# Kernel tuning notes

Measured on AMD Instinct MI355X. Metric: run time of the kernel, lower is better.

## Reference

```python
import jax, jax.numpy as jnp
import numpy as np

N, R, E, DIN, DOUT = 100000, 4, 160000, 128, 128
NEG_SLOPE = 0.2


def setup_inputs() -> dict:
    key = jax.random.key(0)
    ks = jax.random.split(key, 9)
    s_in = 1.0 / np.sqrt(DIN)
    x = jax.random.normal(ks[0], (N, DIN), jnp.float32)
    edge_src = jax.random.randint(ks[1], (R, E), 0, N)
    edge_dst = jax.random.randint(ks[2], (R, E), 0, N)
    # per-relation GATConv params (num_heads=1): fc_src, fc_dst, attn_l, attn_r, bias
    W_src = jax.random.normal(ks[3], (R, DIN, DOUT), jnp.float32) * s_in
    W_dst = jax.random.normal(ks[4], (R, DIN, DOUT), jnp.float32) * s_in
    attn_l = jax.random.normal(ks[5], (R, DOUT), jnp.float32) * 0.1
    attn_r = jax.random.normal(ks[6], (R, DOUT), jnp.float32) * 0.1
    gat_bias = jax.random.normal(ks[7], (R, DOUT), jnp.float32) * 0.01
    h_bias = jnp.zeros((DOUT,), jnp.float32)
    return {"x": x, "edge_src": edge_src, "edge_dst": edge_dst,
            "W_src": W_src, "W_dst": W_dst, "attn_l": attn_l,
            "attn_r": attn_r, "gat_bias": gat_bias, "h_bias": h_bias}


def reference(x, edge_src, edge_dst, W_src, W_dst, attn_l, attn_r, gat_bias, h_bias):
    n = x.shape[0]
    r, e = edge_src.shape
    # per-relation linear projections (GATConv fc_src / fc_dst, no bias)
    hs = jnp.einsum('nd,rde->rne', x, W_src)            # [R,N,D] source messages
    hd = jnp.einsum('nd,rde->rne', x, W_dst)            # [R,N,D] dst attn features
    el = jnp.sum(hs * attn_l[:, None, :], axis=-1)      # [R,N]
    er = jnp.sum(hd * attn_r[:, None, :], axis=-1)      # [R,N]
    rid = jnp.arange(r)[:, None]                        # [R,1]
    # edge attention logits
    logits = jax.nn.leaky_relu(
        jnp.take_along_axis(el, edge_src, axis=1)
        + jnp.take_along_axis(er, edge_dst, axis=1), NEG_SLOPE)  # [R,E]
    # edge softmax grouped by (relation, dst node): flatten into R*N segments
    seg = (edge_dst + rid * n).reshape(-1)              # [R*E]
    lf = logits.reshape(-1)
    m = jax.ops.segment_max(lf, seg, num_segments=r * n)
    a = jnp.exp(lf - m[seg])
    denom = jax.ops.segment_sum(a, seg, num_segments=r * n)
    alpha = a / denom[seg]                              # segment-normalized, denom>=1 at max edge
    msg = alpha[:, None] * hs[rid, edge_src].reshape(r * e, -1)  # [R*E,D]
    agg = jax.ops.segment_sum(msg, seg, num_segments=r * n).reshape(r, n, -1)
    agg = agg + gat_bias[:, None, :]                    # GATConv bias per relation
    h = agg.sum(0) + h_bias                             # HeteroGraphConv 'sum' + h_bias
    return jax.nn.relu(h)                               # activation; dropout eval = id; mean over 1 head = squeeze
```

## Files before the change

### kernel.cpp

```cpp
#include <hip/hip_runtime.h>
#include <hip/hip_bf16.h>

#define N_NODES 100000
#define R_REL 4
#define E_EDGES 160000
#define D 128
#define NEG_SLOPE 0.2f
#define CAP 32

typedef unsigned short u16x8 __attribute__((ext_vector_type(8)));
typedef unsigned short u16x4 __attribute__((ext_vector_type(4)));
typedef __bf16 bf16x8v __attribute__((ext_vector_type(8)));
typedef float f32x4 __attribute__((ext_vector_type(4)));

__device__ inline unsigned short f2bf(float f) {
    unsigned u = __float_as_uint(f);
    return (unsigned short)((u + 0x7FFFu + ((u >> 16) & 1u)) >> 16);
}
__device__ inline float bf2f(unsigned short h) {
    return __uint_as_float(((unsigned)h) << 16);
}

__global__ __launch_bounds__(512) void k_prep2(const float* __restrict__ Wsrc,
        const float* __restrict__ Wdst, const float* __restrict__ al,
        const float* __restrict__ ar, const float* __restrict__ gb,
        const float* __restrict__ hb, float* __restrict__ wl,
        float* __restrict__ wr, float* __restrict__ btot,
        unsigned short* __restrict__ Wt, unsigned* __restrict__ cnt) {
    int b = blockIdx.x, t = threadIdx.x;
    if (b == 0) {
        int r = t >> 7, d = t & 127;
        const float* as = al + r * D;
        const float* ad = ar + r * D;
        const float* rs = Wsrc + (r * D + d) * D;
        const float* rd = Wdst + (r * D + d) * D;
        float s0 = 0.f, s1 = 0.f;
        for (int e = 0; e < D; e++) { s0 += rs[e] * as[e]; s1 += rd[e] * ad[e]; }
        wl[r * D + d] = s0; wr[r * D + d] = s1;
        if (t < D) {
            float bb = hb[t];
            for (int r2 = 0; r2 < R_REL; r2++) bb += gb[r2 * D + t];
            btot[t] = bb;
        }
    } else if (b <= 32) {
        int base = (b - 1) * 2048 + t;
        #pragma unroll
        for (int i = 0; i < 4; i++) {
            int idx = base + i * 512;
            int r = idx >> 14; int rem = idx & 16383; int e = rem >> 7; int k = rem & 127;
            Wt[idx] = f2bf(Wsrc[(r * D + k) * D + e]);
        }
    } else {
        int i = (b - 33) * 512 + t;
        if (i < N_NODES) cnt[i] = 0u;
    }
}

__global__ __launch_bounds__(256) void k_scores_cast(const float* __restrict__ x,
        const float* __restrict__ wl, const float* __restrict__ wr,
        unsigned short* __restrict__ xb, float* __restrict__ el, float* __restrict__ er) {
    __shared__ float swl[R_REL * D], swr[R_REL * D];
    int t = threadIdx.x;
    for (int i = t; i < R_REL * D; i += 256) { swl[i] = wl[i]; swr[i] = wr[i]; }
    __syncthreads();
    int wv = t >> 6, lane = t & 63;
    int half = lane >> 5, q = lane & 31;
    long n = (long)blockIdx.x * 8 + wv * 2 + half;
    float4 v = ((const float4*)(x + n * D))[q];
    u16x4 ov;
    ov[0] = f2bf(v.x); ov[1] = f2bf(v.y); ov[2] = f2bf(v.z); ov[3] = f2bf(v.w);
    *(u16x4*)(xb + n * D + q * 4) = ov;
    float accl[R_REL], accr[R_REL];
    #pragma unroll
    for (int r = 0; r < R_REL; r++) {
        float4 w = ((const float4*)(swl + r * D))[q];
        accl[r] = v.x * w.x + v.y * w.y + v.z * w.z + v.w * w.w;
        float4 u = ((const float4*)(swr + r * D))[q];
        accr[r] = v.x * u.x + v.y * u.y + v.z * u.z + v.w * u.w;
    }
    #pragma unroll
    for (int r = 0; r < R_REL; r++) {
        #pragma unroll
        for (int d = 16; d >= 1; d >>= 1) {
            accl[r] += __shfl_xor(accl[r], d);
            accr[r] += __shfl_xor(accr[r], d);
        }
    }
    if (q == 0) {
        #pragma unroll
        for (int r = 0; r < R_REL; r++) {
            el[r * N_NODES + n] = accl[r];
            er[r * N_NODES + n] = accr[r];
        }
    }
}

__global__ __launch_bounds__(512) void k_gemm(const unsigned short* __restrict__ xb,
                                              const unsigned short* __restrict__ Wt,
                                              unsigned short* __restrict__ hs) {
    __shared__ unsigned short B[D][D + 8];
    int tid = threadIdx.x;
    int w = tid >> 6, l = tid & 63;
    int row16 = l & 15, kgrp = l >> 4;
    int r = blockIdx.y;
    int n0 = blockIdx.x * 256;
    bf16x8v a[2][4];
    int nr[2];
    #pragma unroll
    for (int rf = 0; rf < 2; rf++) {
        int nrow = n0 + w * 32 + rf * 16 + row16;
        nr[rf] = nrow;
        int nc = nrow < N_NODES ? nrow : N_NODES - 1;
        #pragma unroll
        for (int kf = 0; kf < 4; kf++)
            a[rf][kf] = *(const bf16x8v*)(xb + (long)nc * D + kf * 32 + kgrp * 8);
    }
    const unsigned short* Wr = Wt + r * D * D;
    #pragma unroll
    for (int it = 0; it < 4; it++) {
        int fi = (it * 512 + tid) * 8;
        *(u16x8*)(&B[fi >> 7][fi & 127]) = *(const u16x8*)(Wr + fi);
    }
    __syncthreads();
    f32x4 acc[2][8];
    #pragma unroll
    for (int rf = 0; rf < 2; rf++)
        #pragma unroll
        for (int et = 0; et < 8; et++) {
            acc[rf][et][0] = 0.f; acc[rf][et][1] = 0.f;
            acc[rf][et][2] = 0.f; acc[rf][et][3] = 0.f;
        }
    #pragma unroll
    for (int kf = 0; kf < 4; kf++) {
        #pragma unroll
        for (int et = 0; et < 8; et++) {
            bf16x8v av = *(const bf16x8v*)(&B[et * 16 + row16][kf * 32 + kgrp * 8]);
            acc[0][et] = __builtin_amdgcn_mfma_f32_16x16x32_bf16(av, a[0][kf], acc[0][et], 0, 0, 0);
            acc[1][et] = __builtin_amdgcn_mfma_f32_16x16x32_bf16(av, a[1][kf], acc[1][et], 0, 0, 0);
        }
    }
    #pragma unroll
    for (int rf = 0; rf < 2; rf++) {
        if (nr[rf] < N_NODES) {
            unsigned short* orow = hs + ((long)r * N_NODES + nr[rf]) * D;
            #pragma unroll
            for (int et = 0; et < 8; et++) {
                u16x4 o;
                o[0] = f2bf(acc[rf][et][0]); o[1] = f2bf(acc[rf][et][1]);
                o[2] = f2bf(acc[rf][et][2]); o[3] = f2bf(acc[rf][et][3]);
                *(u16x4*)(orow + et * 16 + kgrp * 4) = o;
            }
        }
    }
}

__global__ void k_scatter(const int* __restrict__ esrc, const int* __restrict__ edst,
                          const float* __restrict__ el, const float* __restrict__ er,
                          unsigned* __restrict__ cnt, int2* __restrict__ eb) {
    int e = blockIdx.x * 256 + threadIdx.x;
    if (e >= E_EDGES) return;
    int r = blockIdx.y;
    int t = r * E_EDGES + e;
    int src = esrc[t], dst = edst[t];
    float lg = el[r * N_NODES + src] + er[r * N_NODES + dst];
    lg = lg > 0.f ? lg : NEG_SLOPE * lg;
    float p = __expf(lg);
    unsigned pos = atomicAdd(cnt + dst, 1u);
    if (pos < CAP) eb[dst * CAP + pos] = make_int2(r * N_NODES + src, __float_as_int(p));
}

__global__ __launch_bounds__(256) void k_agg(const int2* __restrict__ eb,
                                             const unsigned* __restrict__ cnt,
                                             const unsigned short* __restrict__ hs,
                                             const float* __restrict__ btot,
                                             float* __restrict__ out) {
    int wv = threadIdx.x >> 6, lane = threadIdx.x & 63;
    int half = lane >> 5, l32 = lane & 31;
    int dst = blockIdx.x * 8 + wv * 2 + half;
    unsigned num = cnt[dst];
    if (num > CAP) num = CAP;
    int rowid = 0, r = 0;
    float p = 0.f;
    if (l32 < num) {
        int2 m = eb[dst * CAP + l32];
        rowid = m.x;
        p = __int_as_float(m.y);
        r = (int)((unsigned)rowid / (unsigned)N_NODES);
    }
    float denom[R_REL];
    #pragma unroll
    for (int rr = 0; rr < R_REL; rr++) {
        float v = (r == rr) ? p : 0.f;
        #pragma unroll
        for (int d = 1; d < 32; d <<= 1) v += __shfl_xor(v, d, 32);
        denom[rr] = v;
    }
    float alpha = (l32 < num) ? p / denom[r] : 0.f;
    int slot2 = l32 >> 4, c16 = lane & 15;
    float acc[8] = {0.f, 0.f, 0.f, 0.f, 0.f, 0.f, 0.f, 0.f};
    unsigned numo = __shfl_xor(num, 32);
    unsigned numMax = num > numo ? num : numo;
    unsigned iters = (numMax + 1) >> 1;
    for (unsigned i = 0; i < iters; i++) {
        unsigned q = slot2 + i * 2;
        int src = half * 32 + (int)q;
        int rid = __shfl(rowid, src);
        float al = __shfl(alpha, src);
        if (q < num) {
            u16x8 v = *(const u16x8*)(hs + (long)rid * D + c16 * 8);
            #pragma unroll
            for (int j = 0; j < 8; j++) acc[j] += al * bf2f(v[j]);
        }
    }
    #pragma unroll
    for (int j = 0; j < 8; j++) acc[j] += __shfl_xor(acc[j], 16);
    if (slot2 == 0) {
        const float4 b0 = *(const float4*)(btot + c16 * 8);
        const float4 b1 = *(const float4*)(btot + c16 * 8 + 4);
        float4 o0, o1;
        o0.x = acc[0] + b0.x; o0.y = acc[1] + b0.y; o0.z = acc[2] + b0.z; o0.w = acc[3] + b0.w;
        o1.x = acc[4] + b1.x; o1.y = acc[5] + b1.y; o1.z = acc[6] + b1.z; o1.w = acc[7] + b1.w;
        o0.x = o0.x > 0.f ? o0.x : 0.f; o0.y = o0.y > 0.f ? o0.y : 0.f;
        o0.z = o0.z > 0.f ? o0.z : 0.f; o0.w = o0.w > 0.f ? o0.w : 0.f;
        o1.x = o1.x > 0.f ? o1.x : 0.f; o1.y = o1.y > 0.f ? o1.y : 0.f;
        o1.z = o1.z > 0.f ? o1.z : 0.f; o1.w = o1.w > 0.f ? o1.w : 0.f;
        *(float4*)(out + (long)dst * D + c16 * 8) = o0;
        *(float4*)(out + (long)dst * D + c16 * 8 + 4) = o1;
    }
}

extern "C" void kernel_launch(void* const* d_in, const int* in_sizes, int n_in,
                              void* d_out, int out_size, void* d_ws, size_t ws_size,
                              hipStream_t stream) {
    const float* x    = (const float*)d_in[0];
    const int*   esrc = (const int*)d_in[1];
    const int*   edst = (const int*)d_in[2];
    const float* Wsrc = (const float*)d_in[3];
    const float* Wdst = (const float*)d_in[4];
    const float* al   = (const float*)d_in[5];
    const float* ar   = (const float*)d_in[6];
    const float* gb   = (const float*)d_in[7];
    const float* hb   = (const float*)d_in[8];
    float* out = (float*)d_out;

    char* ws = (char*)d_ws;
    size_t o = 0;
    auto alloc = [&](size_t bytes) -> char* {
        char* r = ws + o; o += (bytes + 255) & ~(size_t)255; return r;
    };
    unsigned short* xb  = (unsigned short*)alloc((size_t)N_NODES * D * 2);
    unsigned short* hsb = (unsigned short*)alloc((size_t)R_REL * N_NODES * D * 2);
    unsigned short* Wt  = (unsigned short*)alloc((size_t)R_REL * D * D * 2);
    float* el   = (float*)alloc((size_t)R_REL * N_NODES * 4);
    float* er   = (float*)alloc((size_t)R_REL * N_NODES * 4);
    float* wl   = (float*)alloc(R_REL * D * 4);
    float* wr   = (float*)alloc(R_REL * D * 4);
    float* btot = (float*)alloc(D * 4);
    unsigned* cnt = (unsigned*)alloc((size_t)N_NODES * 4);
    int2* eb = (int2*)xb;

    int zblocks = (N_NODES + 511) / 512;
    k_prep2<<<dim3(33 + zblocks), dim3(512), 0, stream>>>(Wsrc, Wdst, al, ar, gb, hb,
                                                          wl, wr, btot, Wt, cnt);
    k_scores_cast<<<dim3(N_NODES / 8), dim3(256), 0, stream>>>(x, wl, wr, xb, el, er);
    k_gemm<<<dim3((N_NODES + 255) / 256, R_REL), dim3(512), 0, stream>>>(xb, Wt, hsb);
    k_scatter<<<dim3((E_EDGES + 255) / 256, R_REL), dim3(256), 0, stream>>>(esrc, edst, el, er, cnt, eb);
    k_agg<<<dim3(N_NODES / 8), dim3(256), 0, stream>>>(eb, cnt, hsb, btot, out);
}
```

Before: 174.3 us.

## Fuse GEMM and edge scatter into one launch with a separate edge buffer

```diff
diff --git a/kernel.cpp b/kernel.cpp
--- a/kernel.cpp
+++ b/kernel.cpp
@@ -7,6 +7,8 @@
 #define D 128
 #define NEG_SLOPE 0.2f
 #define CAP 32
+#define GB 391
+#define SB 313
 
 typedef unsigned short u16x8 __attribute__((ext_vector_type(8)));
 typedef unsigned short u16x4 __attribute__((ext_vector_type(4)));
@@ -95,15 +97,12 @@
     }
 }
 
-__global__ __launch_bounds__(512) void k_gemm(const unsigned short* __restrict__ xb,
-                                              const unsigned short* __restrict__ Wt,
-                                              unsigned short* __restrict__ hs) {
-    __shared__ unsigned short B[D][D + 8];
-    int tid = threadIdx.x;
+__device__ __forceinline__ void gemm_body(int bx, int r, int tid,
+        const unsigned short* __restrict__ xb, const unsigned short* __restrict__ Wt,
+        unsigned short* __restrict__ hs, unsigned short (*B)[D + 8]) {
     int w = tid >> 6, l = tid & 63;
     int row16 = l & 15, kgrp = l >> 4;
-    int r = blockIdx.y;
-    int n0 = blockIdx.x * 256;
+    int n0 = bx * 256;
     bf16x8v a[2][4];
     int nr[2];
     #pragma unroll
@@ -154,12 +153,10 @@
     }
 }
 
-__global__ void k_scatter(const int* __restrict__ esrc, const int* __restrict__ edst,
-                          const float* __restrict__ el, const float* __restrict__ er,
-                          unsigned* __restrict__ cnt, int2* __restrict__ eb) {
-    int e = blockIdx.x * 256 + threadIdx.x;
-    if (e >= E_EDGES) return;
-    int r = blockIdx.y;
+__device__ __forceinline__ void scatter_edge(int e, int r,
+        const int* __restrict__ esrc, const int* __restrict__ edst,
+        const float* __restrict__ el, const float* __restrict__ er,
+        unsigned* __restrict__ cnt, int2* __restrict__ eb) {
     int t = r * E_EDGES + e;
     int src = esrc[t], dst = edst[t];
     float lg = el[r * N_NODES + src] + er[r * N_NODES + dst];
@@ -167,6 +164,37 @@
     float p = __expf(lg);
     unsigned pos = atomicAdd(cnt + dst, 1u);
     if (pos < CAP) eb[dst * CAP + pos] = make_int2(r * N_NODES + src, __float_as_int(p));
+}
+
+__global__ __launch_bounds__(512) void k_gemm_scatter(
+        const unsigned short* __restrict__ xb, const unsigned short* __restrict__ Wt,
+        unsigned short* __restrict__ hs, const int* __restrict__ esrc,
+        const int* __restrict__ edst, const float* __restrict__ el,
+        const float* __restrict__ er, unsigned* __restrict__ cnt,
+        int2* __restrict__ eb) {
+    __shared__ unsigned short B[D][D + 8];
+    int bx = blockIdx.x, r = blockIdx.y, tid = threadIdx.x;
+    if (bx < GB) {
+        gemm_body(bx, r, tid, xb, Wt, hs, B);
+    } else {
+        int e = (bx - GB) * 512 + tid;
+        if (e < E_EDGES) scatter_edge(e, r, esrc, edst, el, er, cnt, eb);
+    }
+}
+
+__global__ __launch_bounds__(512) void k_gemm(const unsigned short* __restrict__ xb,
+                                              const unsigned short* __restrict__ Wt,
+                                              unsigned short* __restrict__ hs) {
+    __shared__ unsigned short B[D][D + 8];
+    gemm_body(blockIdx.x, blockIdx.y, threadIdx.x, xb, Wt, hs, B);
+}
+
+__global__ void k_scatter(const int* __restrict__ esrc, const int* __restrict__ edst,
+                          const float* __restrict__ el, const float* __restrict__ er,
+                          unsigned* __restrict__ cnt, int2* __restrict__ eb) {
+    int e = blockIdx.x * 256 + threadIdx.x;
+    if (e >= E_EDGES) return;
+    scatter_edge(e, blockIdx.y, esrc, edst, el, er, cnt, eb);
 }
 
 __global__ __launch_bounds__(256) void k_agg(const int2* __restrict__ eb,
@@ -203,9 +231,9 @@
     unsigned iters = (numMax + 1) >> 1;
     for (unsigned i = 0; i < iters; i++) {
         unsigned q = slot2 + i * 2;
-        int src = half * 32 + (int)q;
-        int rid = __shfl(rowid, src);
-        float al = __shfl(alpha, src);
+        int srcl = half * 32 + (int)q;
+        int rid = __shfl(rowid, srcl);
+        float al = __shfl(alpha, srcl);
         if (q < num) {
             u16x8 v = *(const u16x8*)(hs + (long)rid * D + c16 * 8);
             #pragma unroll
@@ -257,13 +285,22 @@
     float* wr   = (float*)alloc(R_REL * D * 4);
     float* btot = (float*)alloc(D * 4);
     unsigned* cnt = (unsigned*)alloc((size_t)N_NODES * 4);
-    int2* eb = (int2*)xb;
+    size_t base_end = o;
+    size_t eb_bytes = (size_t)N_NODES * CAP * 8;
+    bool fused = (base_end + eb_bytes) <= ws_size;
+    int2* eb = fused ? (int2*)alloc(eb_bytes) : (int2*)xb;
 
     int zblocks = (N_NODES + 511) / 512;
     k_prep2<<<dim3(33 + zblocks), dim3(512), 0, stream>>>(Wsrc, Wdst, al, ar, gb, hb,
                                                           wl, wr, btot, Wt, cnt);
     k_scores_cast<<<dim3(N_NODES / 8), dim3(256), 0, stream>>>(x, wl, wr, xb, el, er);
-    k_gemm<<<dim3((N_NODES + 255) / 256, R_REL), dim3(512), 0, stream>>>(xb, Wt, hsb);
-    k_scatter<<<dim3((E_EDGES + 255) / 256, R_REL), dim3(256), 0, stream>>>(esrc, edst, el, er, cnt, eb);
+    if (fused) {
+        k_gemm_scatter<<<dim3(GB + SB, R_REL), dim3(512), 0, stream>>>(
+            xb, Wt, hsb, esrc, edst, el, er, cnt, eb);
+    } else {
+        k_gemm<<<dim3(GB, R_REL), dim3(512), 0, stream>>>(xb, Wt, hsb);
+        k_scatter<<<dim3((E_EDGES + 255) / 256, R_REL), dim3(256), 0, stream>>>(
+            esrc, edst, el, er, cnt, eb);
+    }
     k_agg<<<dim3(N_NODES / 8), dim3(256), 0, stream>>>(eb, cnt, hsb, btot, out);
 }
```

Measured after the change: 156.8 us. 1.11x faster.

## Aggregate raw features per relation then project, removing the per-relation GEMM

Applied to the files above, without the earlier changes.

```diff
diff --git a/kernel.cpp b/kernel.cpp
--- a/kernel.cpp
+++ b/kernel.cpp
@@ -7,6 +7,7 @@
 #define D 128
 #define NEG_SLOPE 0.2f
 #define CAP 32
+#define NB_DST 16
 
 typedef unsigned short u16x8 __attribute__((ext_vector_type(8)));
 typedef unsigned short u16x4 __attribute__((ext_vector_type(4)));
@@ -95,65 +96,6 @@
     }
 }
 
-__global__ __launch_bounds__(512) void k_gemm(const unsigned short* __restrict__ xb,
-                                              const unsigned short* __restrict__ Wt,
-                                              unsigned short* __restrict__ hs) {
-    __shared__ unsigned short B[D][D + 8];
-    int tid = threadIdx.x;
-    int w = tid >> 6, l = tid & 63;
-    int row16 = l & 15, kgrp = l >> 4;
-    int r = blockIdx.y;
-    int n0 = blockIdx.x * 256;
-    bf16x8v a[2][4];
-    int nr[2];
-    #pragma unroll
-    for (int rf = 0; rf < 2; rf++) {
-        int nrow = n0 + w * 32 + rf * 16 + row16;
-        nr[rf] = nrow;
-        int nc = nrow < N_NODES ? nrow : N_NODES - 1;
-        #pragma unroll
-        for (int kf = 0; kf < 4; kf++)
-            a[rf][kf] = *(const bf16x8v*)(xb + (long)nc * D + kf * 32 + kgrp * 8);
-    }
-    const unsigned short* Wr = Wt + r * D * D;
-    #pragma unroll
-    for (int it = 0; it < 4; it++) {
-        int fi = (it * 512 + tid) * 8;
-        *(u16x8*)(&B[fi >> 7][fi & 127]) = *(const u16x8*)(Wr + fi);
-    }
-    __syncthreads();
-    f32x4 acc[2][8];
-    #pragma unroll
-    for (int rf = 0; rf < 2; rf++)
-        #pragma unroll
-        for (int et = 0; et < 8; et++) {
-            acc[rf][et][0] = 0.f; acc[rf][et][1] = 0.f;
-            acc[rf][et][2] = 0.f; acc[rf][et][3] = 0.f;
-        }
-    #pragma unroll
-    for (int kf = 0; kf < 4; kf++) {
-        #pragma unroll
-        for (int et = 0; et < 8; et++) {
-            bf16x8v av = *(const bf16x8v*)(&B[et * 16 + row16][kf * 32 + kgrp * 8]);
-            acc[0][et] = __builtin_amdgcn_mfma_f32_16x16x32_bf16(av, a[0][kf], acc[0][et], 0, 0, 0);
-            acc[1][et] = __builtin_amdgcn_mfma_f32_16x16x32_bf16(av, a[1][kf], acc[1][et], 0, 0, 0);
-        }
-    }
-    #pragma unroll
-    for (int rf = 0; rf < 2; rf++) {
-        if (nr[rf] < N_NODES) {
-            unsigned short* orow = hs + ((long)r * N_NODES + nr[rf]) * D;
-            #pragma unroll
-            for (int et = 0; et < 8; et++) {
-                u16x4 o;
-                o[0] = f2bf(acc[rf][et][0]); o[1] = f2bf(acc[rf][et][1]);
-                o[2] = f2bf(acc[rf][et][2]); o[3] = f2bf(acc[rf][et][3]);
-                *(u16x4*)(orow + et * 16 + kgrp * 4) = o;
-            }
-        }
-    }
-}
-
 __global__ void k_scatter(const int* __restrict__ esrc, const int* __restrict__ edst,
                           const float* __restrict__ el, const float* __restrict__ er,
                           unsigned* __restrict__ cnt, int2* __restrict__ eb) {
@@ -169,64 +111,104 @@
     if (pos < CAP) eb[dst * CAP + pos] = make_int2(r * N_NODES + src, __float_as_int(p));
 }
 
-__global__ __launch_bounds__(256) void k_agg(const int2* __restrict__ eb,
-                                             const unsigned* __restrict__ cnt,
-                                             const unsigned short* __restrict__ hs,
-                                             const float* __restrict__ btot,
-                                             float* __restrict__ out) {
-    int wv = threadIdx.x >> 6, lane = threadIdx.x & 63;
+__global__ __launch_bounds__(256) void k_aggproj(
+        const int2* __restrict__ eb, const unsigned* __restrict__ cnt,
+        const unsigned short* __restrict__ xb, const unsigned short* __restrict__ Wt,
+        const float* __restrict__ btot, float* __restrict__ out) {
+    __shared__ unsigned short Z[R_REL][NB_DST][D + 8];
+    int tid = threadIdx.x;
+    int wv = tid >> 6, lane = tid & 63;
     int half = lane >> 5, l32 = lane & 31;
-    int dst = blockIdx.x * 8 + wv * 2 + half;
-    unsigned num = cnt[dst];
-    if (num > CAP) num = CAP;
-    int rowid = 0, r = 0;
-    float p = 0.f;
-    if (l32 < num) {
+    int slot2 = l32 >> 4, c16 = lane & 15;
+    int dbase = blockIdx.x * NB_DST;
+    for (int ps = 0; ps < 2; ps++) {
+        int dloc = wv * 4 + ps * 2 + half;
+        int dst = dbase + dloc;
         int2 m = eb[dst * CAP + l32];
-        rowid = m.x;
-        p = __int_as_float(m.y);
-        r = (int)((unsigned)rowid / (unsigned)N_NODES);
-    }
-    float denom[R_REL];
+        unsigned num = cnt[dst];
+        if (num > CAP) num = CAP;
+        bool live = (unsigned)l32 < num;
+        int rowid = live ? m.x : 0;
+        float pv = live ? __int_as_float(m.y) : 0.f;
+        int r = live ? (int)((unsigned)rowid / (unsigned)N_NODES) : 0;
+        float denom[R_REL];
+        #pragma unroll
+        for (int rr = 0; rr < R_REL; rr++) {
+            float v = (r == rr) ? pv : 0.f;
+            #pragma unroll
+            for (int d = 1; d < 32; d <<= 1) v += __shfl_xor(v, d, 32);
+            denom[rr] = v;
+        }
+        float alpha = live ? pv / denom[r] : 0.f;
+        float accz[R_REL][8];
+        #pragma unroll
+        for (int rr = 0; rr < R_REL; rr++)
+            #pragma unroll
+            for (int j = 0; j < 8; j++) accz[rr][j] = 0.f;
+        unsigned numo = __shfl_xor(num, 32);
+        unsigned numMax = num > numo ? num : numo;
+        unsigned iters = (numMax + 1) >> 1;
+        for (unsigned i = 0; i < iters; i++) {
+            unsigned q = slot2 + i * 2;
+            int srcl = half * 32 + (int)q;
+            int rid = __shfl(rowid, srcl);
+            float al = __shfl(alpha, srcl);
+            if (q < num) {
+                unsigned rr_e = (unsigned)rid / (unsigned)N_NODES;
+                int sidx = rid - (int)(rr_e * (unsigned)N_NODES);
+                u16x8 v = *(const u16x8*)(xb + (long)sidx * D + c16 * 8);
+                #pragma unroll
+                for (int rr = 0; rr < R_REL; rr++) {
+                    float alc = (rr_e == (unsigned)rr) ? al : 0.f;
+                    #pragma unroll
+                    for (int j = 0; j < 8; j++) accz[rr][j] += alc * bf2f(v[j]);
+                }
+            }
+        }
+        #pragma unroll
+        for (int rr = 0; rr < R_REL; rr++)
+            #pragma unroll
+            for (int j = 0; j < 8; j++) accz[rr][j] += __shfl_xor(accz[rr][j], 16);
+        if (slot2 == 0) {
+            #pragma unroll
+            for (int rr = 0; rr < R_REL; rr++) {
+                u16x8 zv;
+                #pragma unroll
+                for (int j = 0; j < 8; j++) zv[j] = f2bf(accz[rr][j]);
+                *(u16x8*)(&Z[rr][dloc][c16 * 8]) = zv;
+            }
+        }
+    }
+    __syncthreads();
+    int row16 = lane & 15, kgrp = lane >> 4;
+    f32x4 acc0, acc1;
+    acc0[0] = 0.f; acc0[1] = 0.f; acc0[2] = 0.f; acc0[3] = 0.f;
+    acc1 = acc0;
     #pragma unroll
     for (int rr = 0; rr < R_REL; rr++) {
-        float v = (r == rr) ? p : 0.f;
-        #pragma unroll
-        for (int d = 1; d < 32; d <<= 1) v += __shfl_xor(v, d, 32);
-        denom[rr] = v;
-    }
-    float alpha = (l32 < num) ? p / denom[r] : 0.f;
-    int slot2 = l32 >> 4, c16 = lane & 15;
-    float acc[8] = {0.f, 0.f, 0.f, 0.f, 0.f, 0.f, 0.f, 0.f};
-    unsigned numo = __shfl_xor(num, 32);
-    unsigned numMax = num > numo ? num : numo;
-    unsigned iters = (numMax + 1) >> 1;
-    for (unsigned i = 0; i < iters; i++) {
-        unsigned q = slot2 + i * 2;
-        int src = half * 32 + (int)q;
-        int rid = __shfl(rowid, src);
-        float al = __shfl(alpha, src);
-        if (q < num) {
-            u16x8 v = *(const u16x8*)(hs + (long)rid * D + c16 * 8);
-            #pragma unroll
-            for (int j = 0; j < 8; j++) acc[j] += al * bf2f(v[j]);
-        }
-    }
-    #pragma unroll
-    for (int j = 0; j < 8; j++) acc[j] += __shfl_xor(acc[j], 16);
-    if (slot2 == 0) {
-        const float4 b0 = *(const float4*)(btot + c16 * 8);
-        const float4 b1 = *(const float4*)(btot + c16 * 8 + 4);
-        float4 o0, o1;
-        o0.x = acc[0] + b0.x; o0.y = acc[1] + b0.y; o0.z = acc[2] + b0.z; o0.w = acc[3] + b0.w;
-        o1.x = acc[4] + b1.x; o1.y = acc[5] + b1.y; o1.z = acc[6] + b1.z; o1.w = acc[7] + b1.w;
-        o0.x = o0.x > 0.f ? o0.x : 0.f; o0.y = o0.y > 0.f ? o0.y : 0.f;
-        o0.z = o0.z > 0.f ? o0.z : 0.f; o0.w = o0.w > 0.f ? o0.w : 0.f;
-        o1.x = o1.x > 0.f ? o1.x : 0.f; o1.y = o1.y > 0.f ? o1.y : 0.f;
-        o1.z = o1.z > 0.f ? o1.z : 0.f; o1.w = o1.w > 0.f ? o1.w : 0.f;
-        *(float4*)(out + (long)dst * D + c16 * 8) = o0;
-        *(float4*)(out + (long)dst * D + c16 * 8 + 4) = o1;
-    }
+        const unsigned short* Wr = Wt + rr * D * D;
+        #pragma unroll
+        for (int kf = 0; kf < 4; kf++) {
+            bf16x8v az = *(const bf16x8v*)(&Z[rr][row16][kf * 32 + kgrp * 8]);
+            bf16x8v av0 = *(const bf16x8v*)(Wr + ((wv * 2) * 16 + row16) * D + kf * 32 + kgrp * 8);
+            bf16x8v av1 = *(const bf16x8v*)(Wr + ((wv * 2 + 1) * 16 + row16) * D + kf * 32 + kgrp * 8);
+            acc0 = __builtin_amdgcn_mfma_f32_16x16x32_bf16(av0, az, acc0, 0, 0, 0);
+            acc1 = __builtin_amdgcn_mfma_f32_16x16x32_bf16(av1, az, acc1, 0, 0, 0);
+        }
+    }
+    float* orow = out + (long)(dbase + row16) * D;
+    int c0 = wv * 32 + kgrp * 4;
+    const float4 b0 = *(const float4*)(btot + c0);
+    const float4 b1 = *(const float4*)(btot + c0 + 16);
+    float4 o0, o1;
+    o0.x = acc0[0] + b0.x; o0.y = acc0[1] + b0.y; o0.z = acc0[2] + b0.z; o0.w = acc0[3] + b0.w;
+    o1.x = acc1[0] + b1.x; o1.y = acc1[1] + b1.y; o1.z = acc1[2] + b1.z; o1.w = acc1[3] + b1.w;
+    o0.x = o0.x > 0.f ? o0.x : 0.f; o0.y = o0.y > 0.f ? o0.y : 0.f;
+    o0.z = o0.z > 0.f ? o0.z : 0.f; o0.w = o0.w > 0.f ? o0.w : 0.f;
+    o1.x = o1.x > 0.f ? o1.x : 0.f; o1.y = o1.y > 0.f ? o1.y : 0.f;
+    o1.z = o1.z > 0.f ? o1.z : 0.f; o1.w = o1.w > 0.f ? o1.w : 0.f;
+    *(float4*)(orow + c0) = o0;
+    *(float4*)(orow + c0 + 16) = o1;
 }
 
 extern "C" void kernel_launch(void* const* d_in, const int* in_sizes, int n_in,
@@ -249,7 +231,6 @@
         char* r = ws + o; o += (bytes + 255) & ~(size_t)255; return r;
     };
     unsigned short* xb  = (unsigned short*)alloc((size_t)N_NODES * D * 2);
-    unsigned short* hsb = (unsigned short*)alloc((size_t)R_REL * N_NODES * D * 2);
     unsigned short* Wt  = (unsigned short*)alloc((size_t)R_REL * D * D * 2);
     float* el   = (float*)alloc((size_t)R_REL * N_NODES * 4);
     float* er   = (float*)alloc((size_t)R_REL * N_NODES * 4);
@@ -257,13 +238,12 @@
     float* wr   = (float*)alloc(R_REL * D * 4);
     float* btot = (float*)alloc(D * 4);
     unsigned* cnt = (unsigned*)alloc((size_t)N_NODES * 4);
-    int2* eb = (int2*)xb;
+    int2* eb = (int2*)alloc((size_t)N_NODES * CAP * 8);
 
     int zblocks = (N_NODES + 511) / 512;
     k_prep2<<<dim3(33 + zblocks), dim3(512), 0, stream>>>(Wsrc, Wdst, al, ar, gb, hb,
                                                           wl, wr, btot, Wt, cnt);
     k_scores_cast<<<dim3(N_NODES / 8), dim3(256), 0, stream>>>(x, wl, wr, xb, el, er);
-    k_gemm<<<dim3((N_NODES + 255) / 256, R_REL), dim3(512), 0, stream>>>(xb, Wt, hsb);
-    k_scatter<<<dim3((E_EDGES + 255) / 256, R_REL), dim3(256), 0, stream>>>(esrc, edst, el, er, cnt, eb);
-    k_agg<<<dim3(N_NODES / 8), dim3(256), 0, stream>>>(eb, cnt, hsb, btot, out);
-}
+    k_scatter<<<dim3(E_EDGES / 256, R_REL), dim3(256), 0, stream>>>(esrc, edst, el, er, cnt, eb);
+    k_aggproj<<<dim3(N_NODES / NB_DST), dim3(256), 0, stream>>>(eb, cnt, xb, Wt, btot, out);
+}
```

Result: slower. 213.8 us (+22.7%).
